# Performance work log

Hardware: AMD Instinct MI355X
Metric: run time of the kernel (lower is better)

The kernel has to match this reference:

```python
import jax, jax.numpy as jnp
import numpy as np

N_NODES = 100000
N_EDGES = 1000000
D_IN = 64
D_OUT = 64
K_HOPS = 3


def setup_inputs() -> dict:
    key = jax.random.key(0)
    k1, k2, k3 = jax.random.split(key, 3)
    x = jax.random.normal(k1, (N_NODES, D_IN), dtype=jnp.float32)
    edge_index = jax.random.randint(k2, (2, N_EDGES), 0, N_NODES, dtype=jnp.int64)
    # Linear layer params (PyG Linear: y = x @ W.T + b)
    W = jax.random.normal(k3, (D_OUT, D_IN), dtype=jnp.float32) * (1.0 / np.sqrt(D_IN))
    b = jnp.zeros((D_OUT,), dtype=jnp.float32)
    return {"x": x, "edge_index": edge_index, "W": W, "b": b}


def reference(x, edge_index, W, b):
    # SGConv: x' = (D^{-1/2} (A + I) D^{-1/2})^K x, then Linear.
    N = x.shape[0]
    src, dst = edge_index[0], edge_index[1]
    loop = jnp.arange(N, dtype=edge_index.dtype)
    src = jnp.concatenate([src, loop])  # add self loops
    dst = jnp.concatenate([dst, loop])
    ones = jnp.ones(src.shape[0], dtype=x.dtype)
    deg = jax.ops.segment_sum(ones, dst, num_segments=N)  # in-degree incl. self loop
    dinv = jnp.where(deg > 0, jax.lax.rsqrt(deg), jnp.zeros_like(deg))
    norm = dinv[src] * dinv[dst]  # [E+N]
    for _ in range(K_HOPS):
        # out[dst] += norm * x[src]
        x = jax.ops.segment_sum(norm[:, None] * x[src], dst, num_segments=N)
    return x @ W.T + b
```

## Files before the change

kernel.cpp:

```cpp
#include <hip/hip_runtime.h>

#define NN 100000
#define NE 1000000
#define D  64
#define CAP 32
#define OVF_CAP 16384

#define FILL_EPT 8
#define FILL_CHUNK (256 * FILL_EPT)
#define FILL_NCHUNK ((NE + FILL_CHUNK - 1) / FILL_CHUNK)
#define PART_SZ 12500
#define SELCAP 512

__device__ __forceinline__ unsigned bf16rne(float f) {
    unsigned h = __float_as_uint(f);
    return (h + 0x7fffu + ((h >> 16) & 1u)) >> 16;
}
__device__ __forceinline__ uint2 pack4(float4 v) {
    uint2 o;
    o.x = bf16rne(v.x) | (bf16rne(v.y) << 16);
    o.y = bf16rne(v.z) | (bf16rne(v.w) << 16);
    return o;
}
__device__ __forceinline__ float4 unpack4(uint2 u) {
    float4 f;
    f.x = __uint_as_float(u.x << 16);
    f.y = __uint_as_float(u.x & 0xffff0000u);
    f.z = __uint_as_float(u.y << 16);
    f.w = __uint_as_float(u.y & 0xffff0000u);
    return f;
}

__global__ void k_cvt(const float2* __restrict__ x2, unsigned* __restrict__ xb,
                      int* __restrict__ cnt, int* __restrict__ ovf_n) {
    int i = blockIdx.x * blockDim.x + threadIdx.x;
    unsigned long long v = __builtin_nontemporal_load((const unsigned long long*)&x2[i]);
    float vx = __uint_as_float((unsigned)(v & 0xffffffffu));
    float vy = __uint_as_float((unsigned)(v >> 32));
    xb[i] = bf16rne(vx) | (bf16rne(vy) << 16);
    if (i < NN) cnt[i] = 0;
    if (i == 0) *ovf_n = 0;
}

__global__ __launch_bounds__(256) void k_fill_bucket(const int* __restrict__ src,
                                                     const int* __restrict__ dst,
                                                     int* __restrict__ cnt,
                                                     int* __restrict__ bucket,
                                                     int* __restrict__ ovf_n,
                                                     int2* __restrict__ ovf) {
    __shared__ int nsel;
    __shared__ int2 sel[SELCAP];
    const int part = blockIdx.x & 7;
    const int lo = part * PART_SZ, hi = lo + PART_SZ;
    const int base = (blockIdx.x >> 3) * FILL_CHUNK + threadIdx.x;

    if (threadIdx.x == 0) nsel = 0;
    __syncthreads();

    #pragma unroll
    for (int it = 0; it < FILL_EPT; ++it) {
        int e = base + it * 256;
        int d = (e < NE) ? __builtin_nontemporal_load(&dst[e]) : -1;
        if (d >= lo && d < hi) {
            int s = __builtin_nontemporal_load(&src[e]);
            int slot = atomicAdd(&nsel, 1);
            if (slot < SELCAP) {
                sel[slot] = make_int2(s, d);
            } else {
                int c = atomicAdd(&cnt[d], 1);
                if (c < CAP) bucket[(size_t)d * CAP + c] = s;
                else { int i = atomicAdd(ovf_n, 1); if (i < OVF_CAP) ovf[i] = make_int2(s, d); }
            }
        }
    }
    __syncthreads();

    int m = min(nsel, SELCAP);
    for (int i = threadIdx.x; i < m; i += 256) {
        int2 p = sel[i];
        int c = atomicAdd(&cnt[p.y], 1);
        if (c < CAP) bucket[(size_t)p.y * CAP + c] = p.x;
        else { int j = atomicAdd(ovf_n, 1); if (j < OVF_CAP) ovf[j] = make_int2(p.x, p.y); }
    }
}


__global__ __launch_bounds__(256) void k_gather_bf16(const uint2* __restrict__ in2,
                                                     const int* __restrict__ cnt,
                                                     const int* __restrict__ bucket,
                                                     const int* __restrict__ ovf_n,
                                                     const int2* __restrict__ ovf,
                                                     uint2* __restrict__ out2) {
    const int tid = threadIdx.x;
    const int l = tid & 15;
    const int n = blockIdx.x * 16 + (tid >> 4);

    const int cn = cnt[n];
    const int deg = min(cn, CAP);
    const float dn = rsqrtf((float)(cn + 1));

    float4 a0 = unpack4(in2[(size_t)n * 16 + l]);
    a0.x *= dn; a0.y *= dn; a0.z *= dn; a0.w *= dn;
    float4 a1 = make_float4(0.f, 0.f, 0.f, 0.f);
    float4 a2 = make_float4(0.f, 0.f, 0.f, 0.f);
    float4 a3 = make_float4(0.f, 0.f, 0.f, 0.f);

    if (deg > 0) {
        int   iA = (l < deg) ? l : 0;
        int   sA = bucket[(size_t)n * CAP + iA];
        float wA = rsqrtf((float)(cnt[sA] + 1));
        const int kmax = deg < 16 ? deg : 16;
        int k = 0;
        for (; k + 3 < kmax; k += 4) {
            int   s0 = __shfl(sA, k + 0, 16);
            int   s1 = __shfl(sA, k + 1, 16);
            int   s2 = __shfl(sA, k + 2, 16);
            int   s3 = __shfl(sA, k + 3, 16);
            float w0 = __shfl(wA, k + 0, 16);
            float w1 = __shfl(wA, k + 1, 16);
            float w2 = __shfl(wA, k + 2, 16);
            float w3 = __shfl(wA, k + 3, 16);
            float4 r0 = unpack4(in2[(size_t)s0 * 16 + l]);
            float4 r1 = unpack4(in2[(size_t)s1 * 16 + l]);
            float4 r2 = unpack4(in2[(size_t)s2 * 16 + l]);
            float4 r3 = unpack4(in2[(size_t)s3 * 16 + l]);
            a0.x = fmaf(w0, r0.x, a0.x); a0.y = fmaf(w0, r0.y, a0.y);
            a0.z = fmaf(w0, r0.z, a0.z); a0.w = fmaf(w0, r0.w, a0.w);
            a1.x = fmaf(w1, r1.x, a1.x); a1.y = fmaf(w1, r1.y, a1.y);
            a1.z = fmaf(w1, r1.z, a1.z); a1.w = fmaf(w1, r1.w, a1.w);
            a2.x = fmaf(w2, r2.x, a2.x); a2.y = fmaf(w2, r2.y, a2.y);
            a2.z = fmaf(w2, r2.z, a2.z); a2.w = fmaf(w2, r2.w, a2.w);
            a3.x = fmaf(w3, r3.x, a3.x); a3.y = fmaf(w3, r3.y, a3.y);
            a3.z = fmaf(w3, r3.z, a3.z); a3.w = fmaf(w3, r3.w, a3.w);
        }
        for (; k < kmax; ++k) {
            int   s0 = __shfl(sA, k, 16);
            float w0 = __shfl(wA, k, 16);
            float4 r0 = unpack4(in2[(size_t)s0 * 16 + l]);
            a0.x = fmaf(w0, r0.x, a0.x); a0.y = fmaf(w0, r0.y, a0.y);
            a0.z = fmaf(w0, r0.z, a0.z); a0.w = fmaf(w0, r0.w, a0.w);
        }
        if (deg > 16) {
            int   iB = (16 + l < deg) ? (16 + l) : 0;
            int   sB = bucket[(size_t)n * CAP + iB];
            float wB = rsqrtf((float)(cnt[sB] + 1));
            const int k2max = deg - 16;
            int k2 = 0;
            for (; k2 + 1 < k2max; k2 += 2) {
                int   s0 = __shfl(sB, k2 + 0, 16);
                int   s1 = __shfl(sB, k2 + 1, 16);
                float w0 = __shfl(wB, k2 + 0, 16);
                float w1 = __shfl(wB, k2 + 1, 16);
                float4 r0 = unpack4(in2[(size_t)s0 * 16 + l]);
                float4 r1 = unpack4(in2[(size_t)s1 * 16 + l]);
                a1.x = fmaf(w0, r0.x, a1.x); a1.y = fmaf(w0, r0.y, a1.y);
                a1.z = fmaf(w0, r0.z, a1.z); a1.w = fmaf(w0, r0.w, a1.w);
                a2.x = fmaf(w1, r1.x, a2.x); a2.y = fmaf(w1, r1.y, a2.y);
                a2.z = fmaf(w1, r1.z, a2.z); a2.w = fmaf(w1, r1.w, a2.w);
            }
            if (k2 < k2max) {
                int   s0 = __shfl(sB, k2, 16);
                float w0 = __shfl(wB, k2, 16);
                float4 r0 = unpack4(in2[(size_t)s0 * 16 + l]);
                a3.x = fmaf(w0, r0.x, a3.x); a3.y = fmaf(w0, r0.y, a3.y);
                a3.z = fmaf(w0, r0.z, a3.z); a3.w = fmaf(w0, r0.w, a3.w);
            }
        }
    }

    int m = *ovf_n;
    if (m > 0) {
        if (m > OVF_CAP) m = OVF_CAP;
        for (int i = 0; i < m; ++i) {
            int2 p = ovf[i];
            if (p.y == n) {
                float w = rsqrtf((float)(cnt[p.x] + 1));
                float4 r = unpack4(in2[(size_t)p.x * 16 + l]);
                a0.x = fmaf(w, r.x, a0.x); a0.y = fmaf(w, r.y, a0.y);
                a0.z = fmaf(w, r.z, a0.z); a0.w = fmaf(w, r.w, a0.w);
            }
        }
    }

    float4 r;
    r.x = dn * ((a0.x + a1.x) + (a2.x + a3.x));
    r.y = dn * ((a0.y + a1.y) + (a2.y + a3.y));
    r.z = dn * ((a0.z + a1.z) + (a2.z + a3.z));
    r.w = dn * ((a0.w + a1.w) + (a2.w + a3.w));
    out2[(size_t)n * 16 + l] = pack4(r);
}

__global__ __launch_bounds__(256) void k_linear_reg(const unsigned short* __restrict__ inb,
                                                    const float* __restrict__ W,
                                                    const float* __restrict__ bias,
                                                    float* __restrict__ out) {
    const int lane = threadIdx.x & 63;
    const int wid  = (blockIdx.x * blockDim.x + threadIdx.x) >> 6;
    const int nw   = (gridDim.x * blockDim.x) >> 6;

    float w[64];
    const float4* W4 = (const float4*)W;
    #pragma unroll
    for (int i = 0; i < 16; ++i) {
        float4 q = W4[lane * 16 + i];
        w[4 * i + 0] = q.x; w[4 * i + 1] = q.y;
        w[4 * i + 2] = q.z; w[4 * i + 3] = q.w;
    }
    const float bo = bias[lane];

    for (int n = wid; n < NN; n += nw) {
        unsigned short rh = __builtin_nontemporal_load(&inb[(size_t)n * 64 + lane]);
        int rli = (int)((unsigned)rh << 16);
        float y0 = bo, y1 = 0.f;
        #pragma unroll
        for (int i = 0; i < 64; i += 2) {
            y0 = fmaf(__int_as_float(__builtin_amdgcn_readlane(rli, i)),     w[i],     y0);
            y1 = fmaf(__int_as_float(__builtin_amdgcn_readlane(rli, i + 1)), w[i + 1], y1);
        }
        __builtin_nontemporal_store(y0 + y1, &out[(size_t)n * 64 + lane]);
    }
}


__global__ void k_init_deg(float* __restrict__ deg) {
    int n = blockIdx.x * blockDim.x + threadIdx.x;
    if (n < NN) deg[n] = 1.0f;
}
__global__ void k_count_deg(const int* __restrict__ dst, float* __restrict__ deg) {
    int e = blockIdx.x * blockDim.x + threadIdx.x;
    if (e < NE) atomicAdd(&deg[dst[e]], 1.0f);
}
__global__ void k_dinv_f(float* __restrict__ deg) {
    int n = blockIdx.x * blockDim.x + threadIdx.x;
    if (n < NN) deg[n] = rsqrtf(deg[n]);
}
__global__ void k_prop_init(const float* __restrict__ in, const float* __restrict__ dinv,
                            float* __restrict__ out) {
    int i = blockIdx.x * blockDim.x + threadIdx.x;
    if (i < NN * D) {
        int n = i >> 6;
        float di = dinv[n];
        out[i] = di * di * in[i];
    }
}
__global__ __launch_bounds__(256) void k_prop_edges(const float* __restrict__ in,
                                                    const int* __restrict__ src,
                                                    const int* __restrict__ dst,
                                                    const float* __restrict__ dinv,
                                                    float* __restrict__ out) {
    int t = blockIdx.x * blockDim.x + threadIdx.x;
    int e = t >> 6, f = t & 63;
    if (e < NE) {
        int s = src[e], d = dst[e];
        float w = dinv[s] * dinv[d];
        atomicAdd(&out[d * D + f], w * in[s * D + f]);
    }
}
__global__ __launch_bounds__(256) void k_linear(const float* __restrict__ in,
                                                const float* __restrict__ W,
                                                const float* __restrict__ bias,
                                                float* __restrict__ out) {
    __shared__ float Wt[64 * 65];
    __shared__ float rows[4][64];
    const int tid = threadIdx.x;
    for (int m = tid; m < 64 * 64; m += 256) {
        int o = m >> 6, i = m & 63;
        Wt[i * 65 + o] = W[m];
    }
    __syncthreads();
    const int wave = tid >> 6, lane = tid & 63;
    const float bo = bias[lane];
    for (int base = blockIdx.x * 4; base < NN; base += gridDim.x * 4) {
        int n = base + wave;
        if (n < NN) {
            rows[wave][lane] = in[n * D + lane];
            float acc = bo;
            #pragma unroll
            for (int i = 0; i < 64; ++i)
                acc = fmaf(rows[wave][i], Wt[i * 65 + lane], acc);
            out[n * D + lane] = acc;
        }
    }
}


extern "C" void kernel_launch(void* const* d_in, const int* in_sizes, int n_in,
                              void* d_out, int out_size, void* d_ws, size_t ws_size,
                              hipStream_t stream) {
    const float* x   = (const float*)d_in[0];
    const int*   ei  = (const int*)d_in[1];
    const float* W   = (const float*)d_in[2];
    const float* b   = (const float*)d_in[3];
    float* out = (float*)d_out;

    const int* src = ei;
    const int* dst = ei + NE;

    char* ws = (char*)d_ws;
    size_t off = 0;
    auto take = [&](size_t bytes) -> char* {
        char* p = ws + off;
        off = (off + bytes + 255) & ~(size_t)255;
        return p;
    };

    int*      cnt    = (int*)take((size_t)NN * 4);
    float*    dinv   = (float*)take((size_t)NN * 4);
    int*      ovf_n  = (int*)take(256);
    int2*     ovf    = (int2*)take((size_t)OVF_CAP * 8);
    unsigned* P      = (unsigned*)take((size_t)NN * 32 * 4);
    unsigned* Q      = (unsigned*)take((size_t)NN * 32 * 4);
    int*      bucket = (int*)take((size_t)NN * CAP * 4);
    float*    buf    = (float*)P;
    const bool use_bucket = (off <= ws_size);

    const int B = 256;
    const int gridE1 = (NE + B - 1) / B;
    const int gridN1 = (NN + B - 1) / B;
    const int gridNW = NN / 16;

    if (use_bucket) {
        k_cvt<<<12500, B, 0, stream>>>((const float2*)x, P, cnt, ovf_n);
        k_fill_bucket<<<FILL_NCHUNK * 8, B, 0, stream>>>(src, dst, cnt, bucket, ovf_n, ovf);

        k_gather_bf16<<<gridNW, B, 0, stream>>>((const uint2*)P, cnt, bucket, ovf_n, ovf, (uint2*)Q);
        k_gather_bf16<<<gridNW, B, 0, stream>>>((const uint2*)Q, cnt, bucket, ovf_n, ovf, (uint2*)P);
        k_gather_bf16<<<gridNW, B, 0, stream>>>((const uint2*)P, cnt, bucket, ovf_n, ovf, (uint2*)Q);
        k_linear_reg<<<1024, B, 0, stream>>>((const unsigned short*)Q, W, b, out);
    } else {
        const int gridF = (NN * D + B - 1) / B;
        const int gridEW = (NE * 64) / B;
        k_init_deg <<<gridN1, B, 0, stream>>>(dinv);
        k_count_deg<<<gridE1, B, 0, stream>>>(dst, dinv);
        k_dinv_f   <<<gridN1, B, 0, stream>>>(dinv);
        k_prop_init <<<gridF, B, 0, stream>>>(x, dinv, buf);
        k_prop_edges<<<gridEW, B, 0, stream>>>(x, src, dst, dinv, buf);
        k_prop_init <<<gridF, B, 0, stream>>>(buf, dinv, out);
        k_prop_edges<<<gridEW, B, 0, stream>>>(buf, src, dst, dinv, out);
        k_prop_init <<<gridF, B, 0, stream>>>(out, dinv, buf);
        k_prop_edges<<<gridEW, B, 0, stream>>>(out, src, dst, dinv, buf);
        k_linear<<<NN / 4, B, 0, stream>>>(buf, W, b, out);
    }
}
```

Before: 179.9 us.

## Fuse bf16 conversion with bucket fill and drop shared-memory staging

Merges the x-to-bf16 conversion kernel and the edge bucket-fill kernel into one launch, with the first block range converting features and the rest filling buckets. Counter zeroing moves to a hipMemsetAsync over a contiguous cnt/ovf_n region, which is reordered in the workspace so the two are adjacent. The fill path drops the shared-memory selection staging and instead loads all 8 edges into registers and then issues global atomics directly. This saves a launch and a block-wide barrier, but adds a memset call and sends all atomics straight to global memory.

```diff
diff --git a/kernel.cpp b/kernel.cpp
--- a/kernel.cpp
+++ b/kernel.cpp
@@ -9,8 +9,8 @@
 #define FILL_EPT 8
 #define FILL_CHUNK (256 * FILL_EPT)
 #define FILL_NCHUNK ((NE + FILL_CHUNK - 1) / FILL_CHUNK)
+#define NCVT 12500
 #define PART_SZ 12500
-#define SELCAP 512
 
 __device__ __forceinline__ unsigned bf16rne(float f) {
     unsigned h = __float_as_uint(f);
@@ -31,56 +31,48 @@
     return f;
 }
 
-__global__ void k_cvt(const float2* __restrict__ x2, unsigned* __restrict__ xb,
-                      int* __restrict__ cnt, int* __restrict__ ovf_n) {
-    int i = blockIdx.x * blockDim.x + threadIdx.x;
-    unsigned long long v = __builtin_nontemporal_load((const unsigned long long*)&x2[i]);
-    float vx = __uint_as_float((unsigned)(v & 0xffffffffu));
-    float vy = __uint_as_float((unsigned)(v >> 32));
-    xb[i] = bf16rne(vx) | (bf16rne(vy) << 16);
-    if (i < NN) cnt[i] = 0;
-    if (i == 0) *ovf_n = 0;
-}
-
-__global__ __launch_bounds__(256) void k_fill_bucket(const int* __restrict__ src,
-                                                     const int* __restrict__ dst,
-                                                     int* __restrict__ cnt,
-                                                     int* __restrict__ bucket,
-                                                     int* __restrict__ ovf_n,
-                                                     int2* __restrict__ ovf) {
-    __shared__ int nsel;
-    __shared__ int2 sel[SELCAP];
-    const int part = blockIdx.x & 7;
+__global__ __launch_bounds__(256) void k_cvt_fill(const float2* __restrict__ x2,
+                                                  unsigned* __restrict__ xb,
+                                                  const int* __restrict__ src,
+                                                  const int* __restrict__ dst,
+                                                  int* __restrict__ cnt,
+                                                  int* __restrict__ bucket,
+                                                  int* __restrict__ ovf_n,
+                                                  int2* __restrict__ ovf) {
+    int bid = blockIdx.x;
+    if (bid < NCVT) {
+        int i = bid * 256 + threadIdx.x;
+        unsigned long long v = __builtin_nontemporal_load((const unsigned long long*)&x2[i]);
+        float vx = __uint_as_float((unsigned)(v & 0xffffffffu));
+        float vy = __uint_as_float((unsigned)(v >> 32));
+        xb[i] = bf16rne(vx) | (bf16rne(vy) << 16);
+        return;
+    }
+    bid -= NCVT;
+    const int part = bid & 7;
     const int lo = part * PART_SZ, hi = lo + PART_SZ;
-    const int base = (blockIdx.x >> 3) * FILL_CHUNK + threadIdx.x;
-
-    if (threadIdx.x == 0) nsel = 0;
-    __syncthreads();
-
+    const int base = (bid >> 3) * FILL_CHUNK + threadIdx.x;
+
+    int ds[FILL_EPT], ss[FILL_EPT];
     #pragma unroll
     for (int it = 0; it < FILL_EPT; ++it) {
         int e = base + it * 256;
         int d = (e < NE) ? __builtin_nontemporal_load(&dst[e]) : -1;
-        if (d >= lo && d < hi) {
-            int s = __builtin_nontemporal_load(&src[e]);
-            int slot = atomicAdd(&nsel, 1);
-            if (slot < SELCAP) {
-                sel[slot] = make_int2(s, d);
+        bool m = (d >= lo && d < hi);
+        ds[it] = m ? d : -1;
+        ss[it] = m ? __builtin_nontemporal_load(&src[e]) : 0;
+    }
+    #pragma unroll
+    for (int it = 0; it < FILL_EPT; ++it) {
+        if (ds[it] >= 0) {
+            int c = atomicAdd(&cnt[ds[it]], 1);
+            if (c < CAP) {
+                bucket[ds[it] * CAP + c] = ss[it];
             } else {
-                int c = atomicAdd(&cnt[d], 1);
-                if (c < CAP) bucket[(size_t)d * CAP + c] = s;
-                else { int i = atomicAdd(ovf_n, 1); if (i < OVF_CAP) ovf[i] = make_int2(s, d); }
+                int i = atomicAdd(ovf_n, 1);
+                if (i < OVF_CAP) ovf[i] = make_int2(ss[it], ds[it]);
             }
         }
-    }
-    __syncthreads();
-
-    int m = min(nsel, SELCAP);
-    for (int i = threadIdx.x; i < m; i += 256) {
-        int2 p = sel[i];
-        int c = atomicAdd(&cnt[p.y], 1);
-        if (c < CAP) bucket[(size_t)p.y * CAP + c] = p.x;
-        else { int j = atomicAdd(ovf_n, 1); if (j < OVF_CAP) ovf[j] = make_int2(p.x, p.y); }
     }
 }
 
@@ -305,8 +297,8 @@
     };
 
     int*      cnt    = (int*)take((size_t)NN * 4);
+    int*      ovf_n  = (int*)take(256);
     float*    dinv   = (float*)take((size_t)NN * 4);
-    int*      ovf_n  = (int*)take(256);
     int2*     ovf    = (int2*)take((size_t)OVF_CAP * 8);
     unsigned* P      = (unsigned*)take((size_t)NN * 32 * 4);
     unsigned* Q      = (unsigned*)take((size_t)NN * 32 * 4);
@@ -320,9 +312,11 @@
     const int gridNW = NN / 16;
 
     if (use_bucket) {
-        k_cvt<<<12500, B, 0, stream>>>((const float2*)x, P, cnt, ovf_n);
-        k_fill_bucket<<<FILL_NCHUNK * 8, B, 0, stream>>>(src, dst, cnt, bucket, ovf_n, ovf);
-
+        size_t zlen = (size_t)((char*)ovf_n - (char*)cnt) + 256;
+        hipMemsetAsync(cnt, 0, zlen, stream);
+        k_cvt_fill<<<NCVT + FILL_NCHUNK * 8, B, 0, stream>>>((const float2*)x, P,
+                                                             src, dst, cnt, bucket,
+                                                             ovf_n, ovf);
         k_gather_bf16<<<gridNW, B, 0, stream>>>((const uint2*)P, cnt, bucket, ovf_n, ovf, (uint2*)Q);
         k_gather_bf16<<<gridNW, B, 0, stream>>>((const uint2*)Q, cnt, bucket, ovf_n, ovf, (uint2*)P);
         k_gather_bf16<<<gridNW, B, 0, stream>>>((const uint2*)P, cnt, bucket, ovf_n, ovf, (uint2*)Q);
```

After: 174.4 us. 3.1% less time.
